# Kernel tuning notes

Hardware: AMD Instinct MI355X
Metric: run time of the kernel (lower is better)

## Reference

```python
import jax, jax.numpy as jnp
import numpy as np

N = 50000
E = 800000
C_IN = 32
C_OUT = 32
K = 8  # number of branch MLPs


def setup_inputs() -> dict:
    key = jax.random.key(0)
    ks = jax.random.split(key, 12)
    x = jax.random.normal(ks[0], (N, C_IN), dtype=jnp.float32)
    pos = jax.random.normal(ks[1], (N, 2), dtype=jnp.float32)
    edge_index = jax.random.randint(ks[2], (2, E), 0, N, dtype=jnp.int32)
    edge_attr = jax.random.normal(ks[3], (E, 4), dtype=jnp.float32)
    edge_weight = jax.random.uniform(ks[4], (E,), dtype=jnp.float32)
    s1 = 1.0 / np.sqrt(C_IN + 4)
    s2 = 1.0 / np.sqrt(C_OUT)
    W1 = jax.random.uniform(ks[5], (K, C_IN + 4, C_OUT), jnp.float32, -s1, s1)
    b1 = jax.random.uniform(ks[6], (K, C_OUT), jnp.float32, -s1, s1)
    W2 = jax.random.uniform(ks[7], (K, C_OUT, C_OUT), jnp.float32, -s2, s2)
    b2 = jax.random.uniform(ks[8], (K, C_OUT), jnp.float32, -s2, s2)
    sr = 1.0 / np.sqrt(C_IN)
    Wr = jax.random.uniform(ks[9], (C_IN, C_OUT), jnp.float32, -sr, sr)
    br = jax.random.uniform(ks[10], (C_OUT,), jnp.float32, -sr, sr)
    return {"x": x, "pos": pos, "edge_index": edge_index, "edge_attr": edge_attr,
            "edge_weight": edge_weight, "W1": W1, "b1": b1, "W2": W2, "b2": b2,
            "Wr": Wr, "br": br}


def reference(x, pos, edge_index, edge_attr, edge_weight, W1, b1, W2, b2, Wr, br):
    src = edge_index[0]  # j (source / neighbor)
    tgt = edge_index[1]  # i (target / aggregation index)

    # gather per-edge features
    x_i = x[tgt]                      # [E, C_IN]
    x_j = x[src]                      # [E, C_IN]
    diff = pos[src] - pos[tgt]        # [E, 2]

    # geometric branch index in [0, 8)
    con0 = (diff[:, 0] > 0).astype(jnp.int32)
    con1 = (diff[:, 1] > 0).astype(jnp.int32)
    con2 = (jnp.abs(diff[:, 0]) - jnp.abs(diff[:, 1]) > 0).astype(jnp.int32)
    idx = con0 + con1 * 2 + con2 * 4  # [E]

    m = jnp.concatenate([x_j - x_i, edge_attr], axis=1)  # [E, C_IN+4]
    # all 8 branch MLPs (Linear->ReLU->Linear->ReLU), then select per edge
    h = jax.nn.relu(jnp.einsum('ec,kcf->ekf', m, W1) + b1[None])   # [E, K, C_OUT]
    f_all = jax.nn.relu(jnp.einsum('ekf,kfg->ekg', h, W2) + b2[None])
    f = jnp.take_along_axis(f_all, idx[:, None, None], axis=1)[:, 0, :]  # [E, C_OUT]
    f = edge_weight[:, None] * f

    # scatter-mean over target nodes
    seg_sum = jax.ops.segment_sum(f, tgt, num_segments=N)
    counts = jax.ops.segment_sum(jnp.ones((f.shape[0],), f.dtype), tgt, num_segments=N)
    out = seg_sum / jnp.maximum(counts, 1.0)[:, None]

    # skip connection
    out = out + x @ Wr + br
    return out
```

## Files before the change

### kernel.cpp

```cpp
#include <hip/hip_runtime.h>

#define N_NODES 50000
#define N_EDGES 800000
#define K_BR    8
#define BCAP    131072
#define MLP_SLOTS (K_BR * BCAP)
#define SCAN_BLOCKS 196
#define BSTRIDE 1024
#define EPT 8
#define P1_BLOCKS 391

typedef _Float16 h2 __attribute__((ext_vector_type(2)));
typedef _Float16 half8 __attribute__((ext_vector_type(8)));
typedef float f32x4 __attribute__((ext_vector_type(4)));

#define MFMA(a, b, c) __builtin_amdgcn_mfma_f32_16x16x32_f16((a), (b), (c), 0, 0, 0)

#define VAL_MASK 0x3FFFFFFFu
#define FLG_A    0x40000000u
#define FLG_P    0x80000000u


__device__ __forceinline__ int branch_idx(float dx, float dy) {
    return (dx > 0.0f ? 1 : 0) + (dy > 0.0f ? 2 : 0) +
           ((fabsf(dx) - fabsf(dy)) > 0.0f ? 4 : 0);
}

__device__ __forceinline__ unsigned pk_f16pair(float a, float b) {
    h2 p; p.x = (_Float16)a; p.y = (_Float16)b;
    return __builtin_bit_cast(unsigned, p);
}

__device__ __forceinline__ unsigned short f16bits(float a) {
    _Float16 h = (_Float16)a;
    return __builtin_bit_cast(unsigned short, h);
}

__global__ void pass1_kernel(const int* __restrict__ ei, const float* __restrict__ pos,
                             const float* __restrict__ ea, const float* __restrict__ ew,
                             const float* __restrict__ x,
                             const float* __restrict__ W1, const float* __restrict__ W2,
                             int* __restrict__ cnt, int* __restrict__ bucketCur,
                             uint4* __restrict__ payload, unsigned* __restrict__ xh,
                             uint4* __restrict__ w1f4, uint4* __restrict__ w2f4) {
    __shared__ int h[K_BR];
    __shared__ int base[K_BR];
    int t = threadIdx.x;
    int tid = blockIdx.x * 256 + t;
    if (t < K_BR) h[t] = 0;

    if (tid < 2048) {
        int L = tid & 63, fl = tid >> 6;
        int nt = fl & 1, kt = (fl >> 1) & 1, k = fl >> 2;
        int quad = L >> 4, col = L & 15;
        unsigned dw[4];
#pragma unroll
        for (int i = 0; i < 4; ++i) {
            float v0 = 0.0f, v1 = 0.0f;
            int k0 = kt * 32 + quad * 8 + 2 * i;
            if (k0 < 36)     v0 = W1[k * 1152 + k0 * 32 + nt * 16 + col];
            if (k0 + 1 < 36) v1 = W1[k * 1152 + (k0 + 1) * 32 + nt * 16 + col];
            dw[i] = pk_f16pair(v0, v1);
        }
        w1f4[tid] = make_uint4(dw[0], dw[1], dw[2], dw[3]);
    } else if (tid < 3072) {
        int u2 = tid - 2048;
        int L = u2 & 63, fl = u2 >> 6;
        int nt = fl & 1, k = fl >> 1;
        int quad = L >> 4, col = L & 15;
        unsigned dw[4];
#pragma unroll
        for (int i = 0; i < 4; ++i) {
            int k0 = quad * 8 + 2 * i;
            dw[i] = pk_f16pair(W2[k * 1024 + k0 * 32 + nt * 16 + col],
                               W2[k * 1024 + (k0 + 1) * 32 + nt * 16 + col]);
        }
        w2f4[u2] = make_uint4(dw[0], dw[1], dw[2], dw[3]);
    }

    __syncthreads();

    int eBase = blockIdx.x * (256 * EPT);
    int sA[EPT], dA[EPT], krA[EPT], slA[EPT];
#pragma unroll
    for (int it = 0; it < EPT; ++it) {
        int e = eBase + it * 256 + t;
        int s = 0, d = 0, k = 0, rank = 0, slot = 0;
        if (e < N_EDGES) {
            s = ei[e]; d = ei[N_EDGES + e];
            float2 ps2 = ((const float2*)pos)[s];
            float2 pd2 = ((const float2*)pos)[d];
            k = branch_idx(ps2.x - pd2.x, ps2.y - pd2.y);
            rank = atomicAdd(&h[k], 1);
            slot = atomicAdd(&cnt[d], 1);
            float2 xv = ((const float2*)x)[e];
            xh[e] = pk_f16pair(xv.x, xv.y);
        }
        sA[it] = s; dA[it] = d; krA[it] = (k << 16) | rank; slA[it] = slot;
    }
    __syncthreads();
    if (t < K_BR) base[t] = (h[t] > 0) ? atomicAdd(&bucketCur[t * BSTRIDE], h[t]) : 0;
    __syncthreads();
#pragma unroll
    for (int it = 0; it < EPT; ++it) {
        int e = eBase + it * 256 + t;
        if (e < N_EDGES) {
            int k = krA[it] >> 16, rank = krA[it] & 0xFFFF;
            float4 eav = ((const float4*)ea)[e];
            unsigned ewh = (unsigned)f16bits(ew[e]);
            int idx = (k << 17) + base[k] + rank;
            payload[idx] = make_uint4((unsigned)sA[it] | ((unsigned)dA[it] << 16),
                                      (unsigned)slA[it] | (ewh << 16),
                                      pk_f16pair(eav.x, eav.y),
                                      pk_f16pair(eav.z, eav.w));
        }
    }
}

__global__ void scan_kernel(const int* __restrict__ cnt, unsigned* __restrict__ ps,
                            int* __restrict__ nodeStart) {
    __shared__ int s[256];
    __shared__ int sh_off;
    int t = threadIdx.x, b = blockIdx.x;
    int i = b * 256 + t;
    int v = (i < N_NODES) ? cnt[i] : 0;
    s[t] = v;
    __syncthreads();
#pragma unroll
    for (int off = 1; off < 256; off <<= 1) {
        int tmp = (t >= off) ? s[t - off] : 0;
        __syncthreads();
        s[t] += tmp;
        __syncthreads();
    }
    int excl = s[t] - v;
    if (t == 255)
        atomicExch(&ps[b], (unsigned)s[255] | (b == 0 ? FLG_P : FLG_A));
    if (t == 0) sh_off = 0;
    if (t < 64 && b > 0) {
        int off = 0;
        int base = b - 1;
        for (;;) {
            int idx = base - t;
            unsigned w = 0;
            if (idx >= 0) {
                do { w = atomicOr(&ps[idx], 0u); } while (!(w & (FLG_A | FLG_P)));
            }
            bool isP = (w & FLG_P) != 0;
            unsigned long long pm = __ballot(isP);
            int firstP = pm ? (__ffsll((unsigned long long)pm) - 1) : 64;
            int contrib = (idx >= 0 && t <= firstP) ? (int)(w & VAL_MASK) : 0;
#pragma unroll
            for (int sh = 32; sh > 0; sh >>= 1) contrib += __shfl_down(contrib, sh, 64);
            contrib = __shfl(contrib, 0, 64);
            off += contrib;
            if (firstP < 64 || base - 64 < 0) break;
            base -= 64;
        }
        if (t == 0) sh_off = off;
    }
    __syncthreads();
    if (i < N_NODES) nodeStart[i] = excl + sh_off;
}

__global__ void __launch_bounds__(64) mlp_kernel(
    const uint4* __restrict__ payload,
    const unsigned* __restrict__ xh,
    const uint4* __restrict__ w1f4, const float* __restrict__ b1,
    const uint4* __restrict__ w2f4, const float* __restrict__ b2,
    const int* __restrict__ nodeStart,
    const int* __restrict__ bucketFill,
    unsigned short* __restrict__ fbuf) {
    __shared__ uint4 lds4[656];
    char* mreg = (char*)lds4;
    char* hreg = mreg + 9216;

    int t = blockIdx.x * 64 + threadIdx.x;
    int u = __builtin_amdgcn_readfirstlane(t);
    int k = u >> 17;
    int fill = bucketFill[k * BSTRIDE];
    if ((u & (BCAP - 1)) >= fill) return;
    int rel = t & (BCAP - 1);
    bool valid = rel < fill;
    int idx = (k << 17) + min(rel, fill - 1);

    int L = threadIdx.x;
    int quad = L >> 4, col = L & 15;

    uint4 pl = payload[idx];
    int s = (int)(pl.x & 0xFFFFu);
    int d = (int)(pl.x >> 16);
    _Float16 wh = __builtin_bit_cast(_Float16, (unsigned short)(pl.y >> 16));
    int slot = valid ? (nodeStart[d] + (int)(pl.y & 0xFFFFu)) : 0;

    const uint4* xj = ((const uint4*)xh) + 4 * (size_t)s;
    const uint4* xi = ((const uint4*)xh) + 4 * (size_t)d;
    uint4* mrow = (uint4*)(mreg + L * 144);
#pragma unroll
    for (int q = 0; q < 4; ++q) {
        half8 a8 = __builtin_bit_cast(half8, xj[q]);
        half8 b8 = __builtin_bit_cast(half8, xi[q]);
        half8 d8 = a8 - b8;
        mrow[q] = __builtin_bit_cast(uint4, d8);
    }
    mrow[4] = make_uint4(pl.z, pl.w, 0u, 0u);
    mrow[5] = make_uint4(0u, 0u, 0u, 0u);
    mrow[6] = make_uint4(0u, 0u, 0u, 0u);
    mrow[7] = make_uint4(0u, 0u, 0u, 0u);

    half8 B1[2][2], B2[2];
#pragma unroll
    for (int kt = 0; kt < 2; ++kt)
#pragma unroll
        for (int nt = 0; nt < 2; ++nt)
            B1[kt][nt] = __builtin_bit_cast(half8, w1f4[((k * 2 + kt) * 2 + nt) * 64 + L]);
#pragma unroll
    for (int nt = 0; nt < 2; ++nt)
        B2[nt] = __builtin_bit_cast(half8, w2f4[(k * 2 + nt) * 64 + L]);
    float b1o0 = b1[k * 32 + col],      b1o1 = b1[k * 32 + 16 + col];
    float b2o0 = b2[k * 32 + col],      b2o1 = b2[k * 32 + 16 + col];

#pragma unroll
    for (int mt = 0; mt < 4; ++mt) {
        int arow = mt * 16 + col;
        half8 a0 = __builtin_bit_cast(half8, *(const uint4*)(mreg + arow * 144 + quad * 16));
        half8 a1 = __builtin_bit_cast(half8, *(const uint4*)(mreg + arow * 144 + 64 + quad * 16));
        f32x4 c0 = {b1o0, b1o0, b1o0, b1o0};
        f32x4 c1 = {b1o1, b1o1, b1o1, b1o1};
        c0 = MFMA(a0, B1[0][0], c0);
        c0 = MFMA(a1, B1[1][0], c0);
        c1 = MFMA(a0, B1[0][1], c1);
        c1 = MFMA(a1, B1[1][1], c1);
#pragma unroll
        for (int r = 0; r < 4; ++r) {
            int er = quad * 4 + r;
            *(unsigned short*)(hreg + er * 80 + col * 2)        = f16bits(fmaxf(c0[r], 0.0f));
            *(unsigned short*)(hreg + er * 80 + (16 + col) * 2) = f16bits(fmaxf(c1[r], 0.0f));
        }
        half8 ah = __builtin_bit_cast(half8, *(const uint4*)(hreg + col * 80 + quad * 16));
        f32x4 d0 = {b2o0, b2o0, b2o0, b2o0};
        f32x4 d1 = {b2o1, b2o1, b2o1, b2o1};
        d0 = MFMA(ah, B2[0], d0);
        d1 = MFMA(ah, B2[1], d1);
#pragma unroll
        for (int r = 0; r < 4; ++r) {
            int edge = mt * 16 + quad * 4 + r;
            *(unsigned short*)(mreg + edge * 144 + col * 2)        = f16bits(fmaxf(d0[r], 0.0f));
            *(unsigned short*)(mreg + edge * 144 + (16 + col) * 2) = f16bits(fmaxf(d1[r], 0.0f));
        }
    }

    half8 w8 = {wh, wh, wh, wh, wh, wh, wh, wh};
    uint4* orow = (uint4*)(mreg + L * 144);
    uint4* frow = (uint4*)(fbuf + 32 * (size_t)slot);
#pragma unroll
    for (int q = 0; q < 4; ++q) {
        half8 v8 = __builtin_bit_cast(half8, orow[q]);
        v8 = v8 * w8;
        if (valid) frow[q] = __builtin_bit_cast(uint4, v8);
    }
}

__global__ void agg_kernel(const unsigned short* __restrict__ fbuf,
                           const int* __restrict__ nodeStart, const int* __restrict__ deg,
                           const float* __restrict__ x, const float* __restrict__ Wr,
                           const float* __restrict__ br, float* __restrict__ out) {
    int t = blockIdx.x * blockDim.x + threadIdx.x;
    if (t >= N_NODES * 8) return;
    int n = t >> 3, g8 = t & 7;
    int st = nodeStart[n], dg = deg[n];
    const uint2* fb = (const uint2*)fbuf;
    float a0 = 0.0f, a1 = 0.0f, a2 = 0.0f, a3 = 0.0f;
    for (int j = 0; j < dg; ++j) {
        uint2 uu = fb[(size_t)(st + j) * 8 + g8];
        h2 p01 = __builtin_bit_cast(h2, uu.x);
        h2 p23 = __builtin_bit_cast(h2, uu.y);
        a0 += (float)p01.x;
        a1 += (float)p01.y;
        a2 += (float)p23.x;
        a3 += (float)p23.y;
    }
    float inv = 1.0f / (float)max(dg, 1);
    int o = g8 * 4;
    a0 = a0 * inv + br[o];
    a1 = a1 * inv + br[o + 1];
    a2 = a2 * inv + br[o + 2];
    a3 = a3 * inv + br[o + 3];
    const float* xr = x + 32 * (size_t)n;
#pragma unroll
    for (int c = 0; c < 32; ++c) {
        float xv = xr[c];
        a0 = fmaf(xv, Wr[c * 32 + o], a0);
        a1 = fmaf(xv, Wr[c * 32 + o + 1], a1);
        a2 = fmaf(xv, Wr[c * 32 + o + 2], a2);
        a3 = fmaf(xv, Wr[c * 32 + o + 3], a3);
    }
    float4* o4 = (float4*)(out + 32 * (size_t)n + o);
    *o4 = make_float4(a0, a1, a2, a3);
}

extern "C" void kernel_launch(void* const* d_in, const int* in_sizes, int n_in,
                              void* d_out, int out_size, void* d_ws, size_t ws_size,
                              hipStream_t stream) {
    const float* x   = (const float*)d_in[0];
    const float* pos = (const float*)d_in[1];
    const int*   ei  = (const int*)d_in[2];
    const float* ea  = (const float*)d_in[3];
    const float* ew  = (const float*)d_in[4];
    const float* W1  = (const float*)d_in[5];
    const float* b1  = (const float*)d_in[6];
    const float* W2  = (const float*)d_in[7];
    const float* b2  = (const float*)d_in[8];
    const float* Wr  = (const float*)d_in[9];
    const float* br  = (const float*)d_in[10];
    float* out = (float*)d_out;

    char* ws = (char*)d_ws;
    unsigned short* fbuf = (unsigned short*)(ws + 0);
    uint4* payload  = (uint4*)(ws + 51200000);
    int* cnt        = (int*)(ws + 67977216);
    int* bucketCur  = (int*)(ws + 68177216);
    unsigned* psLb  = (unsigned*)(ws + 68209984);
    int* nodeStart  = (int*)(ws + 68210816);
    uint4* w1f4     = (uint4*)(ws + 68410816);
    uint4* w2f4     = (uint4*)(ws + 68443584);
    unsigned* xh    = (unsigned*)(ws + 68459968);

    hipMemsetAsync(cnt, 0, 233568, stream);

    pass1_kernel<<<P1_BLOCKS, 256, 0, stream>>>(ei, pos, ea, ew, x, W1, W2,
                                                cnt, bucketCur, payload, xh,
                                                w1f4, w2f4);
    scan_kernel<<<SCAN_BLOCKS, 256, 0, stream>>>(cnt, psLb, nodeStart);
    mlp_kernel<<<MLP_SLOTS / 64, 64, 0, stream>>>(payload, xh, w1f4, b1, w2f4, b2,
                                                  nodeStart, bucketCur, fbuf);
    agg_kernel<<<(N_NODES * 8 + 255) / 256, 256, 0, stream>>>(fbuf, nodeStart, cnt,
                                                              x, Wr, br, out);
}
```

Measured before the change: 196.1 us.

## Replace global per-node atomic slot counting with block-local LDS histograms and column scan

Global atomicAdd on cnt[d], which hands out per-edge slots within each target node, is replaced by a new rank_kernel. In it, 128 blocks each build a 16-bit-packed per-node histogram in shared memory over a contiguous chunk of edges and record each edge's local rank. A colscan_kernel then does a per-node prefix over the 128 block histograms to give block bases and total counts, and pass1 computes the slot as block base plus local rank. The aim is to remove contended global atomics, but it adds two kernels, about 100k shared memory per block, and roughly 25MB of histogram traffic written and read through cntM and blkBase.

```diff
diff --git a/kernel.cpp b/kernel.cpp
--- a/kernel.cpp
+++ b/kernel.cpp
@@ -9,6 +9,8 @@
 #define BSTRIDE 1024
 #define EPT 8
 #define P1_BLOCKS 391
+#define RB 128
+#define RBE 6250
 
 typedef _Float16 h2 __attribute__((ext_vector_type(2)));
 typedef _Float16 half8 __attribute__((ext_vector_type(8)));
@@ -36,19 +38,16 @@
     return __builtin_bit_cast(unsigned short, h);
 }
 
-__global__ void pass1_kernel(const int* __restrict__ ei, const float* __restrict__ pos,
-                             const float* __restrict__ ea, const float* __restrict__ ew,
-                             const float* __restrict__ x,
-                             const float* __restrict__ W1, const float* __restrict__ W2,
-                             int* __restrict__ cnt, int* __restrict__ bucketCur,
-                             uint4* __restrict__ payload, unsigned* __restrict__ xh,
-                             uint4* __restrict__ w1f4, uint4* __restrict__ w2f4) {
-    __shared__ int h[K_BR];
-    __shared__ int base[K_BR];
-    int t = threadIdx.x;
-    int tid = blockIdx.x * 256 + t;
-    if (t < K_BR) h[t] = 0;
-
+__global__ void __launch_bounds__(256) rank_kernel(
+    const int* __restrict__ ei, const float* __restrict__ x,
+    const float* __restrict__ W1, const float* __restrict__ W2,
+    unsigned short* __restrict__ rankB, unsigned short* __restrict__ cntM,
+    unsigned* __restrict__ xh, uint4* __restrict__ w1f4, uint4* __restrict__ w2f4) {
+    __shared__ unsigned hist[N_NODES / 2];
+    int t = threadIdx.x, b = blockIdx.x;
+    for (int i = t; i < N_NODES / 2; i += 256) hist[i] = 0;
+
+    int tid = b * 256 + t;
     if (tid < 2048) {
         int L = tid & 63, fl = tid >> 6;
         int nt = fl & 1, kt = (fl >> 1) & 1, k = fl >> 2;
@@ -78,6 +77,52 @@
         w2f4[u2] = make_uint4(dw[0], dw[1], dw[2], dw[3]);
     }
 
+    __syncthreads();
+    int eb = b * RBE;
+    for (int it = 0; it < (RBE + 255) / 256; ++it) {
+        int r = it * 256 + t;
+        if (r < RBE) {
+            int e = eb + r;
+            int d = ei[N_EDGES + e];
+            unsigned add = (d & 1) ? (1u << 16) : 1u;
+            unsigned old = atomicAdd(&hist[d >> 1], add);
+            unsigned rk = (d & 1) ? (old >> 16) : (old & 0xFFFFu);
+            rankB[e] = (unsigned short)rk;
+            float2 xv = ((const float2*)x)[e];
+            xh[e] = pk_f16pair(xv.x, xv.y);
+        }
+    }
+    __syncthreads();
+    unsigned* cm = (unsigned*)(cntM + (size_t)b * N_NODES);
+    for (int i = t; i < N_NODES / 2; i += 256) cm[i] = hist[i];
+}
+
+__global__ void colscan_kernel(const unsigned short* __restrict__ cntM,
+                               unsigned short* __restrict__ blkBase,
+                               int* __restrict__ cnt) {
+    int d = blockIdx.x * 256 + threadIdx.x;
+    if (d >= N_NODES) return;
+    int acc = 0;
+#pragma unroll 8
+    for (int b = 0; b < RB; ++b) {
+        size_t i = (size_t)b * N_NODES + d;
+        int v = cntM[i];
+        blkBase[i] = (unsigned short)acc;
+        acc += v;
+    }
+    cnt[d] = acc;
+}
+
+__global__ void pass1_kernel(const int* __restrict__ ei, const float* __restrict__ pos,
+                             const float* __restrict__ ea, const float* __restrict__ ew,
+                             const unsigned short* __restrict__ rankB,
+                             const unsigned short* __restrict__ blkBase,
+                             int* __restrict__ bucketCur,
+                             uint4* __restrict__ payload) {
+    __shared__ int h[K_BR];
+    __shared__ int base[K_BR];
+    int t = threadIdx.x;
+    if (t < K_BR) h[t] = 0;
     __syncthreads();
 
     int eBase = blockIdx.x * (256 * EPT);
@@ -92,9 +137,8 @@
             float2 pd2 = ((const float2*)pos)[d];
             k = branch_idx(ps2.x - pd2.x, ps2.y - pd2.y);
             rank = atomicAdd(&h[k], 1);
-            slot = atomicAdd(&cnt[d], 1);
-            float2 xv = ((const float2*)x)[e];
-            xh[e] = pk_f16pair(xv.x, xv.y);
+            int bb = e / RBE;
+            slot = (int)blkBase[(size_t)bb * N_NODES + d] + (int)rankB[e];
         }
         sA[it] = s; dA[it] = d; krA[it] = (k << 16) | rank; slA[it] = slot;
     }
@@ -325,13 +369,17 @@
     uint4* w1f4     = (uint4*)(ws + 68410816);
     uint4* w2f4     = (uint4*)(ws + 68443584);
     unsigned* xh    = (unsigned*)(ws + 68459968);
-
-    hipMemsetAsync(cnt, 0, 233568, stream);
-
-    pass1_kernel<<<P1_BLOCKS, 256, 0, stream>>>(ei, pos, ea, ew, x, W1, W2,
-                                                cnt, bucketCur, payload, xh,
-                                                w1f4, w2f4);
+    unsigned short* rankB   = (unsigned short*)(ws + 71659968);
+    unsigned short* cntM    = (unsigned short*)(ws + 73259968);
+    unsigned short* blkBase = (unsigned short*)(ws + 86059968);
+
+    hipMemsetAsync(bucketCur, 0, 33568, stream);
+
+    rank_kernel<<<RB, 256, 0, stream>>>(ei, x, W1, W2, rankB, cntM, xh, w1f4, w2f4);
+    colscan_kernel<<<SCAN_BLOCKS, 256, 0, stream>>>(cntM, blkBase, cnt);
     scan_kernel<<<SCAN_BLOCKS, 256, 0, stream>>>(cnt, psLb, nodeStart);
+    pass1_kernel<<<P1_BLOCKS, 256, 0, stream>>>(ei, pos, ea, ew, rankB, blkBase,
+                                                bucketCur, payload);
     mlp_kernel<<<MLP_SLOTS / 64, 64, 0, stream>>>(payload, xh, w1f4, b1, w2f4, b2,
                                                   nodeStart, bucketCur, fbuf);
     agg_kernel<<<(N_NODES * 8 + 255) / 256, 256, 0, stream>>>(fbuf, nodeStart, cnt,
```

Result: slower. 203.9 us (+4.0%).
